# Optimization experiments

Hardware: AMD Instinct MI355X
Metric: run time of the kernel (lower is better)

## Reference

```python
import jax, jax.numpy as jnp
import numpy as np

LRELU_ALPHA = 0.2       # LeakyReLU slope (alpha arg of GraphAttentionLayer)
NEG_INF = -9e15         # zero_vec value from the torch code
N1, N2, N3 = 3000, 2500, 2500
IN_F, OUT_F, HEADS = 128, 64, 2


def setup_inputs() -> dict:
    key = jax.random.key(0)
    ks = jax.random.split(key, 13)
    N = N1 + N2 + N3
    h = jax.random.normal(ks[0], (N, IN_F), jnp.float32)
    A1  = jax.random.randint(ks[1],  (N1, N1), 0, 2, jnp.int32)
    A2  = jax.random.randint(ks[2],  (N2, N2), 0, 2, jnp.int32)
    A3  = jax.random.randint(ks[3],  (N3, N3), 0, 2, jnp.int32)
    A12 = jax.random.randint(ks[4],  (N1, N2), 0, 2, jnp.int32)
    A13 = jax.random.randint(ks[5],  (N1, N3), 0, 2, jnp.int32)
    A23 = jax.random.randint(ks[6],  (N2, N3), 0, 2, jnp.int32)
    A21 = jax.random.randint(ks[7],  (N2, N1), 0, 2, jnp.int32)
    A31 = jax.random.randint(ks[8],  (N3, N1), 0, 2, jnp.int32)
    A32 = jax.random.randint(ks[9],  (N3, N2), 0, 2, jnp.int32)
    # per-head GAT parameters (xavier-ish scale)
    Ws = jax.random.normal(ks[10], (HEADS, IN_F, OUT_F), jnp.float32) * 0.12
    a_param = jax.random.normal(ks[11], (HEADS, 2 * OUT_F, 1), jnp.float32) * 0.12
    return dict(h=h, A1=A1, A2=A2, A3=A3, A12=A12, A13=A13, A23=A23,
                A21=A21, A31=A31, A32=A32, Ws=Ws, a_param=a_param)


def reference(h, A1, A2, A3, A12, A13, A23, A21, A31, A32, Ws, a_param):
    n1, n2, n3 = A1.shape[0], A2.shape[0], A3.shape[0]
    # The 9 block assignments in the torch forward tile the full NxN matrix,
    # so they are equivalent to one block-structured mask.
    mask = jnp.block([[A1,  A12, A13],
                      [A21, A2,  A23],
                      [A31, A32, A3]]) > 0          # [N, N] bool

    Wh = jnp.einsum('nf,hfo->hno', h, Ws)           # [H, N, O]
    a1 = a_param[:, :OUT_F, 0]                      # [H, O]
    a2 = a_param[:, OUT_F:, 0]                      # [H, O]
    Wh1 = jnp.einsum('hno,ho->hn', Wh, a1)          # [H, N]
    Wh2 = jnp.einsum('hno,ho->hn', Wh, a2)          # [H, N]
    e = jax.nn.leaky_relu(Wh1[:, :, None] + Wh2[:, None, :], LRELU_ALPHA)  # [H,N,N]
    att = jax.nn.softmax(jnp.where(mask[None], e, NEG_INF), axis=-1)
    # dropout is identity in eval mode
    mid = jnp.einsum('hij,hjo->hio', att, Wh)       # [H, N, O]
    out = jax.nn.elu(mid)                           # concat=True -> elu
    x2 = out.transpose(1, 0, 2).reshape(h.shape[0], -1)  # [N, H*O] head concat

    x3 = jax.nn.log_softmax(x2[n1 + n2:], axis=1)   # group-3 nodes
    x4 = jax.nn.log_softmax(x2[:n1], axis=1)        # group-1 nodes
    x5 = jax.nn.log_softmax(x2[n1:n1 + n2], axis=1) # group-2 nodes
    return (x3, x4, x5)
```

## Files before the change

kernel.cpp:

```cpp
#include <hip/hip_runtime.h>
#include <hip/hip_bf16.h>


#define CN1 3000
#define CN2 2500
#define CN3 2500
#define NTOT 8000
#define INF_ 128
#define OUTF 64
#define LOG2E 1.44269504088896340736f
#define ALPHA 0.2f

typedef __attribute__((ext_vector_type(4))) float f32x4;
typedef __attribute__((ext_vector_type(8))) short short8;
union B16x8 { int4 i4; short8 s8; unsigned int u[4]; };

#if defined(__has_builtin)
#if __has_builtin(__builtin_amdgcn_exp2f)
#define EXP2F(x) __builtin_amdgcn_exp2f(x)
#endif
#endif
#ifndef EXP2F
#define EXP2F(x) exp2f(x)
#endif

__device__ inline float wave_sum(float v) {
  for (int d = 32; d; d >>= 1) v += __shfl_xor(v, d, 64);
  return v;
}

__device__ inline unsigned int pk2(float a, float b) {
  union { __hip_bfloat162 h; unsigned int u; } cv;
  cv.h = __float22bfloat162_rn(make_float2(a, b));
  return cv.u;
}

__device__ inline unsigned int pack2_bf16(float a, float b) {
  unsigned ua = __float_as_uint(a);
  ua = (ua + 0x7FFFu + ((ua >> 16) & 1u)) >> 16;
  unsigned ub = __float_as_uint(b);
  ub = (ub + 0x7FFFu + ((ub >> 16) & 1u)) & 0xFFFF0000u;
  return ub | ua;
}

__global__ __launch_bounds__(256)
void k1_pack_wh(const int* __restrict__ A1,  const int* __restrict__ A12, const int* __restrict__ A13,
                const int* __restrict__ A21, const int* __restrict__ A2,  const int* __restrict__ A23,
                const int* __restrict__ A31, const int* __restrict__ A32, const int* __restrict__ A3,
                const float* __restrict__ hv, const float* __restrict__ Wsv,
                const float* __restrict__ ap,
                unsigned int* __restrict__ packed,
                float* __restrict__ Whf,
                float* __restrict__ Wh1s,
                float* __restrict__ Wh2s) {
  const int bid = blockIdx.x;
  const int widx = threadIdx.x >> 6;
  const int lane = threadIdx.x & 63;

  if (bid < 2000) {
    const int i = bid * 4 + widx;
    const int *p0, *p1, *p2;
    if (i < CN1)            { p0 = A1  + i * CN1;          p1 = A12 + i * CN2;          p2 = A13 + i * CN3; }
    else if (i < CN1 + CN2) { int r = i - CN1;       p0 = A21 + r * CN1; p1 = A2  + r * CN2; p2 = A23 + r * CN3; }
    else                    { int r = i - CN1 - CN2; p0 = A31 + r * CN1; p1 = A32 + r * CN2; p2 = A3  + r * CN3; }
    unsigned int* pkrow = packed + (i >> 4) * 4000 + (i & 15);
#pragma unroll
    for (int it = 0; it < 4; ++it) {
      const int t = it * 64 + lane;
      if (t >= 250) break;
      const int j0 = t * 32;
      unsigned int word = 0;
      if (t != 93 && t != 171) {
        const int* base = (j0 + 32 <= CN1) ? (p0 + j0)
                        : (j0 >= CN1 + CN2) ? (p2 + (j0 - CN1 - CN2))
                                            : (p1 + (j0 - CN1));
        const int4* q = (const int4*)base;
        int4 v[8];
#pragma unroll
        for (int k = 0; k < 8; ++k) v[k] = q[k];
#pragma unroll
        for (int k = 0; k < 8; ++k) {
          word |= (v[k].x > 0 ? 1u : 0u) << (4 * k);
          word |= (v[k].y > 0 ? 1u : 0u) << (4 * k + 1);
          word |= (v[k].z > 0 ? 1u : 0u) << (4 * k + 2);
          word |= (v[k].w > 0 ? 1u : 0u) << (4 * k + 3);
        }
      } else {
#pragma unroll 8
        for (int e = 0; e < 32; ++e) {
          const int j = j0 + e;
          int mval = (j < CN1) ? p0[j]
                   : (j < CN1 + CN2) ? p1[j - CN1]
                                     : p2[j - CN1 - CN2];
          word |= (mval > 0 ? 1u : 0u) << e;
        }
      }
      pkrow[t * 16] = word;
    }
  } else {
    const int o = lane;
    const int n = (bid - 2000) * 4 + widx;
    const float* hrow = hv + n * INF_;
    const float* Ws0 = Wsv + o;
    const float* Ws1 = Wsv + INF_ * OUTF + o;
    float a0a = 0.f, a0b = 0.f, a1a = 0.f, a1b = 0.f;
#pragma unroll 8
    for (int f = 0; f < INF_; f += 2) {
      float h0 = hrow[f], h1 = hrow[f + 1];
      a0a += h0 * Ws0[f * OUTF];
      a0b += h1 * Ws0[(f + 1) * OUTF];
      a1a += h0 * Ws1[f * OUTF];
      a1b += h1 * Ws1[(f + 1) * OUTF];
    }
    float acc0 = a0a + a0b, acc1 = a1a + a1b;
    Whf[(0 * NTOT + n) * OUTF + o] = acc0;
    Whf[(1 * NTOT + n) * OUTF + o] = acc1;
    float s10 = wave_sum(acc0 * ap[o]);
    float s20 = wave_sum(acc0 * ap[OUTF + o]);
    float s11 = wave_sum(acc1 * ap[2 * OUTF + o]);
    float s21 = wave_sum(acc1 * ap[3 * OUTF + o]);
    if (o == 0) {
      Wh1s[n] = s10 * LOG2E;        Wh2s[n] = s20 * LOG2E;
      Wh1s[NTOT + n] = s11 * LOG2E; Wh2s[NTOT + n] = s21 * LOG2E;
    }
  }
}

__global__ __launch_bounds__(256)
void k2_bpack_m2(const float* __restrict__ Whf, const float* __restrict__ Wh2s,
                 int4* __restrict__ WhB, float* __restrict__ M2s) {
  const int bid = blockIdx.x;
  __shared__ float red[4];
  if (bid < 500) {
    const int gid = bid * 256 + threadIdx.x;
    const int lane = gid & 63;
    const int c = (gid >> 6) & 3;
    const int t = (gid >> 8) % 250;
    const int hd = gid / 64000;
    const int jb = t * 32 + (lane >> 4) * 8;
    const int col = c * 16 + (lane & 15);
    const float* src = Whf + (hd * NTOT + jb) * OUTF + col;
    B16x8 out;
#pragma unroll
    for (int e2 = 0; e2 < 4; ++e2)
      out.u[e2] = pack2_bf16(src[(2 * e2) * OUTF], src[(2 * e2 + 1) * OUTF]);
    WhB[gid] = out.i4;
  } else {
    const int hd = bid - 500;
    float mx = -1e30f;
    for (int i = threadIdx.x; i < NTOT; i += 256)
      mx = fmaxf(mx, Wh2s[hd * NTOT + i]);
    for (int d = 32; d; d >>= 1) mx = fmaxf(mx, __shfl_xor(mx, d, 64));
    if ((threadIdx.x & 63) == 0) red[threadIdx.x >> 6] = mx;
    __syncthreads();
    if (threadIdx.x == 0)
      M2s[hd] = fmaxf(fmaxf(red[0], red[1]), fmaxf(red[2], red[3]));
  }
}

__global__ __launch_bounds__(128)
void k_attn_mfma(const unsigned int* __restrict__ packed,
                 const float* __restrict__ Wh1s, const float* __restrict__ Wh2s,
                 const float* __restrict__ M2s, const int4* __restrict__ WhB,
                 float* __restrict__ partAcc,
                 float* __restrict__ partS)
{
  const int widx = threadIdx.x >> 6;
  const int lane = threadIdx.x & 63;
  const int m = lane & 15;
  const int g = lane >> 4;
  const int kb = g * 8;
  const int rowblk = blockIdx.x;
  const int i = rowblk * 16 + m;
  const int jy = blockIdx.y, njy = gridDim.y;
  const int s = jy * 2 + widx, ns = njy * 2;
  const int t0 = (250 * s) / ns, t1 = (250 * (s + 1)) / ns;

  const unsigned int* pkb = packed + rowblk * 4000 + m;

  const float w1s0 = Wh1s[i],        w1s1 = Wh1s[NTOT + i];
  const float y0 = w1s0 + M2s[0],    y1 = w1s1 + M2s[1];
  const float ci0 = fmaxf(y0, ALPHA * y0), ci1 = fmaxf(y1, ALPHA * y1);
  const float a1c0 = w1s0 - ci0, b1c0 = ALPHA * w1s0 - ci0;
  const float a1c1 = w1s1 - ci1, b1c1 = ALPHA * w1s1 - ci1;
  const float* wh2_0 = Wh2s;
  const float* wh2_1 = Wh2s + NTOT;

  f32x4 a0_0 = {0.f,0.f,0.f,0.f}, a0_1 = a0_0, a0_2 = a0_0, a0_3 = a0_0;
  f32x4 a1_0 = a0_0, a1_1 = a0_0, a1_2 = a0_0, a1_3 = a0_0;
  f32x4 s0v = a0_0, s1v = a0_0;

  B16x8 ones;
#pragma unroll
  for (int e2 = 0; e2 < 4; ++e2) ones.u[e2] = 0x3F803F80u;

  struct Frags { int4 f0[4], f1[4]; float4 w0a, w0b, w1a, w1b; };
  auto load_frags = [&](int t, Frags& F) {
    const int4* bp0 = WhB + t * 256 + lane;
    const int4* bp1 = WhB + (250 + t) * 256 + lane;
#pragma unroll
    for (int c = 0; c < 4; ++c) { F.f0[c] = bp0[c * 64]; F.f1[c] = bp1[c * 64]; }
    const float* w0 = wh2_0 + t * 32 + kb;
    const float* w1 = wh2_1 + t * 32 + kb;
    F.w0a = *(const float4*)w0; F.w0b = *(const float4*)(w0 + 4);
    F.w1a = *(const float4*)w1; F.w1b = *(const float4*)(w1 + 4);
  };

  auto compute = [&](unsigned int mw, const Frags& F) {
    const unsigned bits = (mw >> kb) & 0xffu;
    const float w0v[8] = {F.w0a.x, F.w0a.y, F.w0a.z, F.w0a.w, F.w0b.x, F.w0b.y, F.w0b.z, F.w0b.w};
    const float w1v[8] = {F.w1a.x, F.w1a.y, F.w1a.z, F.w1a.w, F.w1b.x, F.w1b.y, F.w1b.z, F.w1b.w};
    float q0[8], q1[8];
#pragma unroll
    for (int e = 0; e < 8; ++e) {
      bool on = ((bits >> e) & 1u) != 0u;
      float xa0 = a1c0 + w0v[e];
      float xb0 = fmaf(ALPHA, w0v[e], b1c0);
      float p0e = EXP2F(fmaxf(xa0, xb0));
      q0[e] = on ? p0e : 0.f;
      float xa1 = a1c1 + w1v[e];
      float xb1 = fmaf(ALPHA, w1v[e], b1c1);
      float p1e = EXP2F(fmaxf(xa1, xb1));
      q1[e] = on ? p1e : 0.f;
    }
    B16x8 af0, af1;
#pragma unroll
    for (int e2 = 0; e2 < 4; ++e2) {
      af0.u[e2] = pk2(q0[2 * e2], q0[2 * e2 + 1]);
      af1.u[e2] = pk2(q1[2 * e2], q1[2 * e2 + 1]);
    }
    B16x8 b;
    b.i4 = F.f0[0]; a0_0 = __builtin_amdgcn_mfma_f32_16x16x32_bf16(af0.s8, b.s8, a0_0, 0, 0, 0);
    b.i4 = F.f0[1]; a0_1 = __builtin_amdgcn_mfma_f32_16x16x32_bf16(af0.s8, b.s8, a0_1, 0, 0, 0);
    b.i4 = F.f0[2]; a0_2 = __builtin_amdgcn_mfma_f32_16x16x32_bf16(af0.s8, b.s8, a0_2, 0, 0, 0);
    b.i4 = F.f0[3]; a0_3 = __builtin_amdgcn_mfma_f32_16x16x32_bf16(af0.s8, b.s8, a0_3, 0, 0, 0);
    s0v = __builtin_amdgcn_mfma_f32_16x16x32_bf16(af0.s8, ones.s8, s0v, 0, 0, 0);
    b.i4 = F.f1[0]; a1_0 = __builtin_amdgcn_mfma_f32_16x16x32_bf16(af1.s8, b.s8, a1_0, 0, 0, 0);
    b.i4 = F.f1[1]; a1_1 = __builtin_amdgcn_mfma_f32_16x16x32_bf16(af1.s8, b.s8, a1_1, 0, 0, 0);
    b.i4 = F.f1[2]; a1_2 = __builtin_amdgcn_mfma_f32_16x16x32_bf16(af1.s8, b.s8, a1_2, 0, 0, 0);
    b.i4 = F.f1[3]; a1_3 = __builtin_amdgcn_mfma_f32_16x16x32_bf16(af1.s8, b.s8, a1_3, 0, 0, 0);
    s1v = __builtin_amdgcn_mfma_f32_16x16x32_bf16(af1.s8, ones.s8, s1v, 0, 0, 0);
  };

  unsigned int mw0 = pkb[t0 * 16];
  unsigned int mw1 = pkb[min(t0 + 1, t1 - 1) * 16];
  Frags Fc, Fn;
  load_frags(t0, Fc);
  for (int t = t0; t < t1; ++t) {
    load_frags(min(t + 1, t1 - 1), Fn);
    unsigned int mw2 = pkb[min(t + 2, t1 - 1) * 16];
    compute(mw0, Fc);
    mw0 = mw1; mw1 = mw2;
    Fc = Fn;
  }

  __shared__ f32x4 lds[10][64];
  if (widx == 1) {
    lds[0][lane] = a0_0; lds[1][lane] = a0_1; lds[2][lane] = a0_2; lds[3][lane] = a0_3;
    lds[4][lane] = a1_0; lds[5][lane] = a1_1; lds[6][lane] = a1_2; lds[7][lane] = a1_3;
    lds[8][lane] = s0v;  lds[9][lane] = s1v;
  }
  __syncthreads();
  if (widx == 0) {
    a0_0 += lds[0][lane]; a0_1 += lds[1][lane]; a0_2 += lds[2][lane]; a0_3 += lds[3][lane];
    a1_0 += lds[4][lane]; a1_1 += lds[5][lane]; a1_2 += lds[6][lane]; a1_3 += lds[7][lane];
    s0v  += lds[8][lane]; s1v  += lds[9][lane];

    const int base0 = (jy * 2 + 0) * NTOT + rowblk * 16;
    const int base1 = (jy * 2 + 1) * NTOT + rowblk * 16;
    if (m == 0) {
#pragma unroll
      for (int q = 0; q < 4; ++q) {
        partS[base0 + g * 4 + q] = s0v[q];
        partS[base1 + g * 4 + q] = s1v[q];
      }
    }
    float* o0 = partAcc + base0 * OUTF;
    float* o1 = partAcc + base1 * OUTF;
#pragma unroll
    for (int q = 0; q < 4; ++q) {
      const int row = g * 4 + q;
      o0[row * OUTF +      m] = a0_0[q];
      o0[row * OUTF + 16 + m] = a0_1[q];
      o0[row * OUTF + 32 + m] = a0_2[q];
      o0[row * OUTF + 48 + m] = a0_3[q];
      o1[row * OUTF +      m] = a1_0[q];
      o1[row * OUTF + 16 + m] = a1_1[q];
      o1[row * OUTF + 32 + m] = a1_2[q];
      o1[row * OUTF + 48 + m] = a1_3[q];
    }
  }
}

__global__ void k_final(const float* __restrict__ partAcc, const float* __restrict__ partS,
                        int njy, float* __restrict__ out) {
  const int wave = threadIdx.x >> 6, lane = threadIdx.x & 63;
  const int n = blockIdx.x * 4 + wave;
  float x[2];
#pragma unroll
  for (int hd = 0; hd < 2; ++hd) {
    float a = 0.f, s = 0.f;
    for (int jy = 0; jy < njy; ++jy) {
      a += partAcc[((jy * 2 + hd) * NTOT + n) * OUTF + lane];
      s += partS[(jy * 2 + hd) * NTOT + n];
    }
    float mid = a / s;
    x[hd] = mid > 0.f ? mid : (__expf(mid) - 1.f);
  }
  float mx = fmaxf(x[0], x[1]);
  for (int d = 32; d; d >>= 1) mx = fmaxf(mx, __shfl_xor(mx, d, 64));
  float se = __expf(x[0] - mx) + __expf(x[1] - mx);
  for (int d = 32; d; d >>= 1) se += __shfl_xor(se, d, 64);
  const float lse = mx + __logf(se);
  const int orow = (n >= CN1 + CN2) ? (n - CN1 - CN2) : (n + CN3);
  out[orow * 128 + lane]      = x[0] - lse;
  out[orow * 128 + 64 + lane] = x[1] - lse;
}

__global__ void k_sentinel(float* __restrict__ out, float v) {
  out[blockIdx.x * 256 + threadIdx.x] = v;
}

extern "C" void kernel_launch(void* const* d_in, const int* in_sizes, int n_in,
                              void* d_out, int out_size, void* d_ws, size_t ws_size,
                              hipStream_t stream) {
  float* outf = (float*)d_out;

  static const int EXP[12] = {1024000, 9000000, 6250000, 6250000, 7500000, 7500000,
                              6250000, 7500000, 7500000, 6250000, 16384, 256};
  bool exact = (n_in == 12);
  if (exact) for (int i = 0; i < 12; ++i) if (in_sizes[i] != EXP[i]) { exact = false; break; }

  const size_t FIXED = 64000 + 64000 + 256 + 2048000 + 8000000;
  int njy = 0;
  for (int cand = 8; cand >= 1; cand >>= 1) {
    size_t need = FIXED + (size_t)cand * 64000 + (size_t)cand * 4096000;
    if (ws_size >= need) { njy = cand; break; }
  }
  if (!exact || njy == 0) {
    k_sentinel<<<dim3(4000), dim3(256), 0, stream>>>(outf, -148.0f);
    return;
  }

  const float* h  = (const float*)d_in[0];
  const int* A1  = (const int*)d_in[1];
  const int* A2  = (const int*)d_in[2];
  const int* A3  = (const int*)d_in[3];
  const int* A12 = (const int*)d_in[4];
  const int* A13 = (const int*)d_in[5];
  const int* A23 = (const int*)d_in[6];
  const int* A21 = (const int*)d_in[7];
  const int* A31 = (const int*)d_in[8];
  const int* A32 = (const int*)d_in[9];
  const float* Ws = (const float*)d_in[10];
  const float* ap = (const float*)d_in[11];

  char* w = (char*)d_ws;
  float*        Wh1s    = (float*)(w);
  float*        Wh2s    = (float*)(w + 64000);
  float*        M2s     = (float*)(w + 128000);
  int4*         WhB     = (int4*) (w + 128256);
  unsigned int* packed  = (unsigned int*)(w + 2176256);
  float*        partS   = (float*)(w + 10176256);
  float*        Whf     = (float*)(w + 10176256 + (size_t)njy * 64000);
  float*        partAcc = Whf;

  k1_pack_wh <<<dim3(4000),     dim3(256), 0, stream>>>(A1, A12, A13, A21, A2, A23, A31, A32, A3,
                                                        h, Ws, ap, packed, Whf, Wh1s, Wh2s);
  k2_bpack_m2<<<dim3(502),      dim3(256), 0, stream>>>(Whf, Wh2s, WhB, M2s);
  k_attn_mfma<<<dim3(500, njy), dim3(128), 0, stream>>>(packed, Wh1s, Wh2s, M2s, WhB,
                                                        partAcc, partS);
  k_final    <<<dim3(2000),     dim3(256), 0, stream>>>(partAcc, partS, njy, outf);
}
```

Baseline: 363.5 us.

## Process attention heads sequentially to cut registers and interleave pack/Wh blocks

The MFMA attention kernel now loops over the two heads one after the other instead of computing both in the same pass. This halves the live accumulators and prefetched fragments, and launch_bounds(128,5) asks the compiler for higher occupancy. In exchange, the mask words are read twice and the loop overhead is doubled. Separately, k1 interleaves mask-packing blocks with Wh-projection blocks (even/odd block ids) so both kinds of work are spread across the GPU.

Result: slower. 397.3 us (+9.3%).

```diff
diff --git a/kernel.cpp b/kernel.cpp
--- a/kernel.cpp
+++ b/kernel.cpp
@@ -54,11 +54,12 @@
                 float* __restrict__ Wh1s,
                 float* __restrict__ Wh2s) {
   const int bid = blockIdx.x;
+  const int half = bid >> 1;
   const int widx = threadIdx.x >> 6;
   const int lane = threadIdx.x & 63;
 
-  if (bid < 2000) {
-    const int i = bid * 4 + widx;
+  if ((bid & 1) == 0) {
+    const int i = half * 4 + widx;
     const int *p0, *p1, *p2;
     if (i < CN1)            { p0 = A1  + i * CN1;          p1 = A12 + i * CN2;          p2 = A13 + i * CN3; }
     else if (i < CN1 + CN2) { int r = i - CN1;       p0 = A21 + r * CN1; p1 = A2  + r * CN2; p2 = A23 + r * CN3; }
@@ -99,7 +100,7 @@
     }
   } else {
     const int o = lane;
-    const int n = (bid - 2000) * 4 + widx;
+    const int n = half * 4 + widx;
     const float* hrow = hv + n * INF_;
     const float* Ws0 = Wsv + o;
     const float* Ws1 = Wsv + INF_ * OUTF + o;
@@ -158,7 +159,7 @@
   }
 }
 
-__global__ __launch_bounds__(128)
+__global__ __launch_bounds__(128, 5)
 void k_attn_mfma(const unsigned int* __restrict__ packed,
                  const float* __restrict__ Wh1s, const float* __restrict__ Wh2s,
                  const float* __restrict__ M2s, const int4* __restrict__ WhB,
@@ -178,116 +179,89 @@
 
   const unsigned int* pkb = packed + rowblk * 4000 + m;
 
-  const float w1s0 = Wh1s[i],        w1s1 = Wh1s[NTOT + i];
-  const float y0 = w1s0 + M2s[0],    y1 = w1s1 + M2s[1];
-  const float ci0 = fmaxf(y0, ALPHA * y0), ci1 = fmaxf(y1, ALPHA * y1);
-  const float a1c0 = w1s0 - ci0, b1c0 = ALPHA * w1s0 - ci0;
-  const float a1c1 = w1s1 - ci1, b1c1 = ALPHA * w1s1 - ci1;
-  const float* wh2_0 = Wh2s;
-  const float* wh2_1 = Wh2s + NTOT;
-
-  f32x4 a0_0 = {0.f,0.f,0.f,0.f}, a0_1 = a0_0, a0_2 = a0_0, a0_3 = a0_0;
-  f32x4 a1_0 = a0_0, a1_1 = a0_0, a1_2 = a0_0, a1_3 = a0_0;
-  f32x4 s0v = a0_0, s1v = a0_0;
-
   B16x8 ones;
 #pragma unroll
   for (int e2 = 0; e2 < 4; ++e2) ones.u[e2] = 0x3F803F80u;
 
-  struct Frags { int4 f0[4], f1[4]; float4 w0a, w0b, w1a, w1b; };
-  auto load_frags = [&](int t, Frags& F) {
-    const int4* bp0 = WhB + t * 256 + lane;
-    const int4* bp1 = WhB + (250 + t) * 256 + lane;
-#pragma unroll
-    for (int c = 0; c < 4; ++c) { F.f0[c] = bp0[c * 64]; F.f1[c] = bp1[c * 64]; }
-    const float* w0 = wh2_0 + t * 32 + kb;
-    const float* w1 = wh2_1 + t * 32 + kb;
-    F.w0a = *(const float4*)w0; F.w0b = *(const float4*)(w0 + 4);
-    F.w1a = *(const float4*)w1; F.w1b = *(const float4*)(w1 + 4);
-  };
-
-  auto compute = [&](unsigned int mw, const Frags& F) {
-    const unsigned bits = (mw >> kb) & 0xffu;
-    const float w0v[8] = {F.w0a.x, F.w0a.y, F.w0a.z, F.w0a.w, F.w0b.x, F.w0b.y, F.w0b.z, F.w0b.w};
-    const float w1v[8] = {F.w1a.x, F.w1a.y, F.w1a.z, F.w1a.w, F.w1b.x, F.w1b.y, F.w1b.z, F.w1b.w};
-    float q0[8], q1[8];
-#pragma unroll
-    for (int e = 0; e < 8; ++e) {
-      bool on = ((bits >> e) & 1u) != 0u;
-      float xa0 = a1c0 + w0v[e];
-      float xb0 = fmaf(ALPHA, w0v[e], b1c0);
-      float p0e = EXP2F(fmaxf(xa0, xb0));
-      q0[e] = on ? p0e : 0.f;
-      float xa1 = a1c1 + w1v[e];
-      float xb1 = fmaf(ALPHA, w1v[e], b1c1);
-      float p1e = EXP2F(fmaxf(xa1, xb1));
-      q1[e] = on ? p1e : 0.f;
-    }
-    B16x8 af0, af1;
-#pragma unroll
-    for (int e2 = 0; e2 < 4; ++e2) {
-      af0.u[e2] = pk2(q0[2 * e2], q0[2 * e2 + 1]);
-      af1.u[e2] = pk2(q1[2 * e2], q1[2 * e2 + 1]);
-    }
-    B16x8 b;
-    b.i4 = F.f0[0]; a0_0 = __builtin_amdgcn_mfma_f32_16x16x32_bf16(af0.s8, b.s8, a0_0, 0, 0, 0);
-    b.i4 = F.f0[1]; a0_1 = __builtin_amdgcn_mfma_f32_16x16x32_bf16(af0.s8, b.s8, a0_1, 0, 0, 0);
-    b.i4 = F.f0[2]; a0_2 = __builtin_amdgcn_mfma_f32_16x16x32_bf16(af0.s8, b.s8, a0_2, 0, 0, 0);
-    b.i4 = F.f0[3]; a0_3 = __builtin_amdgcn_mfma_f32_16x16x32_bf16(af0.s8, b.s8, a0_3, 0, 0, 0);
-    s0v = __builtin_amdgcn_mfma_f32_16x16x32_bf16(af0.s8, ones.s8, s0v, 0, 0, 0);
-    b.i4 = F.f1[0]; a1_0 = __builtin_amdgcn_mfma_f32_16x16x32_bf16(af1.s8, b.s8, a1_0, 0, 0, 0);
-    b.i4 = F.f1[1]; a1_1 = __builtin_amdgcn_mfma_f32_16x16x32_bf16(af1.s8, b.s8, a1_1, 0, 0, 0);
-    b.i4 = F.f1[2]; a1_2 = __builtin_amdgcn_mfma_f32_16x16x32_bf16(af1.s8, b.s8, a1_2, 0, 0, 0);
-    b.i4 = F.f1[3]; a1_3 = __builtin_amdgcn_mfma_f32_16x16x32_bf16(af1.s8, b.s8, a1_3, 0, 0, 0);
-    s1v = __builtin_amdgcn_mfma_f32_16x16x32_bf16(af1.s8, ones.s8, s1v, 0, 0, 0);
-  };
-
-  unsigned int mw0 = pkb[t0 * 16];
-  unsigned int mw1 = pkb[min(t0 + 1, t1 - 1) * 16];
-  Frags Fc, Fn;
-  load_frags(t0, Fc);
-  for (int t = t0; t < t1; ++t) {
-    load_frags(min(t + 1, t1 - 1), Fn);
-    unsigned int mw2 = pkb[min(t + 2, t1 - 1) * 16];
-    compute(mw0, Fc);
-    mw0 = mw1; mw1 = mw2;
-    Fc = Fn;
-  }
-
-  __shared__ f32x4 lds[10][64];
-  if (widx == 1) {
-    lds[0][lane] = a0_0; lds[1][lane] = a0_1; lds[2][lane] = a0_2; lds[3][lane] = a0_3;
-    lds[4][lane] = a1_0; lds[5][lane] = a1_1; lds[6][lane] = a1_2; lds[7][lane] = a1_3;
-    lds[8][lane] = s0v;  lds[9][lane] = s1v;
-  }
-  __syncthreads();
-  if (widx == 0) {
-    a0_0 += lds[0][lane]; a0_1 += lds[1][lane]; a0_2 += lds[2][lane]; a0_3 += lds[3][lane];
-    a1_0 += lds[4][lane]; a1_1 += lds[5][lane]; a1_2 += lds[6][lane]; a1_3 += lds[7][lane];
-    s0v  += lds[8][lane]; s1v  += lds[9][lane];
-
-    const int base0 = (jy * 2 + 0) * NTOT + rowblk * 16;
-    const int base1 = (jy * 2 + 1) * NTOT + rowblk * 16;
-    if (m == 0) {
+  __shared__ f32x4 lds[5][64];
+
+  for (int hd = 0; hd < 2; ++hd) {
+    const float w1s = Wh1s[hd * NTOT + i];
+    const float y = w1s + M2s[hd];
+    const float ci = fmaxf(y, ALPHA * y);
+    const float a1c = w1s - ci, b1c = ALPHA * w1s - ci;
+    const float* wh2 = Wh2s + hd * NTOT;
+    const int4* whb = WhB + hd * 250 * 256;
+
+    f32x4 ac0 = {0.f,0.f,0.f,0.f}, ac1 = ac0, ac2 = ac0, ac3 = ac0, sv = ac0;
+
+    auto load_f = [&](int t, int4* f, float4& wa, float4& wb) {
+      const int4* bp = whb + t * 256 + lane;
+#pragma unroll
+      for (int c = 0; c < 4; ++c) f[c] = bp[c * 64];
+      const float* w = wh2 + t * 32 + kb;
+      wa = *(const float4*)w;
+      wb = *(const float4*)(w + 4);
+    };
+
+    unsigned int mw0 = pkb[t0 * 16];
+    unsigned int mw1 = pkb[min(t0 + 1, t1 - 1) * 16];
+    int4 fc[4], fn[4]; float4 wac, wbc, wan, wbn;
+    load_f(t0, fc, wac, wbc);
+    for (int t = t0; t < t1; ++t) {
+      load_f(min(t + 1, t1 - 1), fn, wan, wbn);
+      unsigned int mw2 = pkb[min(t + 2, t1 - 1) * 16];
+      {
+        const unsigned bits = (mw0 >> kb) & 0xffu;
+        const float wv[8] = {wac.x, wac.y, wac.z, wac.w, wbc.x, wbc.y, wbc.z, wbc.w};
+        float q[8];
+#pragma unroll
+        for (int e = 0; e < 8; ++e) {
+          bool on = ((bits >> e) & 1u) != 0u;
+          float xa = a1c + wv[e];
+          float xb = fmaf(ALPHA, wv[e], b1c);
+          float pe = EXP2F(fmaxf(xa, xb));
+          q[e] = on ? pe : 0.f;
+        }
+        B16x8 af;
+#pragma unroll
+        for (int e2 = 0; e2 < 4; ++e2) af.u[e2] = pk2(q[2 * e2], q[2 * e2 + 1]);
+        B16x8 b;
+        b.i4 = fc[0]; ac0 = __builtin_amdgcn_mfma_f32_16x16x32_bf16(af.s8, b.s8, ac0, 0, 0, 0);
+        b.i4 = fc[1]; ac1 = __builtin_amdgcn_mfma_f32_16x16x32_bf16(af.s8, b.s8, ac1, 0, 0, 0);
+        b.i4 = fc[2]; ac2 = __builtin_amdgcn_mfma_f32_16x16x32_bf16(af.s8, b.s8, ac2, 0, 0, 0);
+        b.i4 = fc[3]; ac3 = __builtin_amdgcn_mfma_f32_16x16x32_bf16(af.s8, b.s8, ac3, 0, 0, 0);
+        sv = __builtin_amdgcn_mfma_f32_16x16x32_bf16(af.s8, ones.s8, sv, 0, 0, 0);
+      }
+      mw0 = mw1; mw1 = mw2;
+#pragma unroll
+      for (int c = 0; c < 4; ++c) fc[c] = fn[c];
+      wac = wan; wbc = wbn;
+    }
+
+    __syncthreads();
+    if (widx == 1) {
+      lds[0][lane] = ac0; lds[1][lane] = ac1; lds[2][lane] = ac2;
+      lds[3][lane] = ac3; lds[4][lane] = sv;
+    }
+    __syncthreads();
+    if (widx == 0) {
+      ac0 += lds[0][lane]; ac1 += lds[1][lane]; ac2 += lds[2][lane];
+      ac3 += lds[3][lane]; sv  += lds[4][lane];
+      const int base = (jy * 2 + hd) * NTOT + rowblk * 16;
+      if (m == 0) {
+#pragma unroll
+        for (int q = 0; q < 4; ++q) partS[base + g * 4 + q] = sv[q];
+      }
+      float* o = partAcc + base * OUTF;
 #pragma unroll
       for (int q = 0; q < 4; ++q) {
-        partS[base0 + g * 4 + q] = s0v[q];
-        partS[base1 + g * 4 + q] = s1v[q];
+        const int row = g * 4 + q;
+        o[row * OUTF +      m] = ac0[q];
+        o[row * OUTF + 16 + m] = ac1[q];
+        o[row * OUTF + 32 + m] = ac2[q];
+        o[row * OUTF + 48 + m] = ac3[q];
       }
-    }
-    float* o0 = partAcc + base0 * OUTF;
-    float* o1 = partAcc + base1 * OUTF;
-#pragma unroll
-    for (int q = 0; q < 4; ++q) {
-      const int row = g * 4 + q;
-      o0[row * OUTF +      m] = a0_0[q];
-      o0[row * OUTF + 16 + m] = a0_1[q];
-      o0[row * OUTF + 32 + m] = a0_2[q];
-      o0[row * OUTF + 48 + m] = a0_3[q];
-      o1[row * OUTF +      m] = a1_0[q];
-      o1[row * OUTF + 16 + m] = a1_1[q];
-      o1[row * OUTF + 32 + m] = a1_2[q];
-      o1[row * OUTF + 48 + m] = a1_3[q];
     }
   }
 }
```
